# Kernel optimization log

Measured on AMD Instinct MI355X. Metric: run time of the kernel, lower is better.

The kernel has to match this reference:

```python
import jax, jax.numpy as jnp
import numpy as np
from math import pi, sqrt, factorial

NUM_SPHERICAL = 7
NUM_RADIAL = 6
CUTOFF = 5.0


def _sph_jn_np(x, n):
    # spherical Bessel j_n(x) in float64 numpy via upward recurrence
    x = np.asarray(x, dtype=np.float64)
    jm = np.sin(x) / x
    if n == 0:
        return jm
    jc = np.sin(x) / x**2 - np.cos(x) / x
    for l in range(2, n + 1):
        jm, jc = jc, (2 * l - 1) / x * jc - jm
    return jc


def _jn_zeros(n, k):
    # first k positive zeros of j_l for l = 0..n-1 (zeros of j_l interleave those of j_{l-1})
    nz = k + n
    z = np.zeros((n, nz))
    z[0] = np.arange(1, nz + 1) * np.pi
    for l in range(1, n):
        for j in range(nz - l):
            a, b = z[l - 1, j], z[l - 1, j + 1]
            fa = _sph_jn_np(a, l)
            for _ in range(100):
                m = 0.5 * (a + b)
                fm = _sph_jn_np(m, l)
                if fa * fm <= 0:
                    b = m
                else:
                    a, fa = m, fm
            z[l, j] = 0.5 * (a + b)
    return z[:, :k]


_ZEROS_NP = _jn_zeros(NUM_SPHERICAL, NUM_RADIAL)  # (n, k)
_NORM_NP = np.array([[(0.5 * _sph_jn_np(_ZEROS_NP[l, j], l + 1) ** 2) ** -0.5
                      for j in range(NUM_RADIAL)] for l in range(NUM_SPHERICAL)])
BESSEL_ZEROS = jnp.asarray(_ZEROS_NP, dtype=jnp.float32)  # z_{l,j}
BESSEL_NORM = jnp.asarray(_NORM_NP, dtype=jnp.float32)    # sqrt(2)/|j_{l+1}(z_{l,j})|


def _rbf(dist):
    # normalized spherical Bessel basis: rbf[:, l*k + j] = norm[l,j] * j_l(z_{l,j} * dist/cutoff)
    d = dist / CUTOFF
    u = d[:, None, None] * BESSEL_ZEROS[None]  # (E, n, k)
    cols = []
    for l in range(NUM_SPHERICAL):
        x = u[:, l, :]
        jm = jnp.sin(x) / x  # j_0
        if l == 0:
            jc = jm
        else:
            jc = jnp.sin(x) / (x * x) - jnp.cos(x) / x  # j_1
        for ll in range(2, l + 1):
            jm, jc = jc, (2 * ll - 1) / x * jc - jm
        cols.append(BESSEL_NORM[l] * jc)
    return jnp.concatenate(cols, axis=1)  # (E, n*k)


def _cbf(angle, phi):
    # real spherical harmonics Y_{l,m}(angle, phi), flat order m = -l..l per l
    n = NUM_SPHERICAL
    z = jnp.cos(angle)
    s = jnp.sin(angle)
    P = {(0, 0): jnp.ones_like(z)}
    for m in range(1, n):
        P[(m, m)] = (1 - 2 * m) * s * P[(m - 1, m - 1)]  # Condon-Shortley phase included
    for m in range(0, n - 1):
        P[(m + 1, m)] = (2 * m + 1) * z * P[(m, m)]
    for m in range(n):
        for l in range(m + 2, n):
            P[(l, m)] = ((2 * l - 1) * z * P[(l - 1, m)] - (l + m - 1) * P[(l - 2, m)]) / (l - m)

    def pref(l, m):
        return sqrt((2 * l + 1) * factorial(l - m) / (4.0 * pi * factorial(l + m)))

    cols = [jnp.full_like(angle, 0.5 / sqrt(pi))]  # Y_00 constant
    for l in range(1, n):
        for m in range(-l, l + 1):
            am = abs(m)
            if m < 0:
                cols.append(sqrt(2.0) * pref(l, am) * jnp.sin(am * phi) * P[(l, am)])
            elif m == 0:
                cols.append(pref(l, 0) * P[(l, 0)])
            else:
                cols.append(sqrt(2.0) * pref(l, am) * jnp.cos(am * phi) * P[(l, am)])
    return jnp.stack(cols, axis=1)  # (T, n*n)


def setup_inputs() -> dict:
    key = jax.random.key(0)
    kd, ka, kp, ki = jax.random.split(key, 4)
    E, T = 150000, 500000
    dist = jax.random.uniform(kd, (E,), minval=0.5, maxval=5.0, dtype=jnp.float32)
    angle = jax.random.uniform(ka, (T,), minval=0.0, maxval=float(np.pi), dtype=jnp.float32)
    phi = jax.random.uniform(kp, (T,), minval=-float(np.pi), maxval=float(np.pi), dtype=jnp.float32)
    idx_kj = jax.random.randint(ki, (T,), 0, E)
    return {"dist": dist, "angle": angle, "phi": phi, "idx_kj": idx_kj}


def reference(dist, angle, phi, idx_kj):
    n, k = NUM_SPHERICAL, NUM_RADIAL
    rbf = _rbf(dist)          # (E, n*k)
    cbf = _cbf(angle, phi)    # (T, n*n)
    out = (rbf[idx_kj].reshape(-1, 1, n, k) * cbf.reshape(-1, n, n, 1)).reshape(-1, n * n * k)
    return out
```

## Files before the change

kernel.cpp:

```cpp
#include <hip/hip_runtime.h>
#include <math.h>

#ifndef M_PI
#define M_PI 3.14159265358979323846
#endif

#define NS 7
#define NK 6
#define GT 64
#define BT 256
#define NC (NS*NS)
#define NR (NS*NK)
#define NF2 147

typedef float f32x2 __attribute__((ext_vector_type(2)));


__device__ double d_sph_jl(double x, int l) {
  double s = sin(x), c = cos(x);
  double j0 = s / x;
  if (l == 0) return j0;
  double j1 = s / (x * x) - c / x;
  for (int ll = 2; ll <= l; ++ll) {
    double t = (2.0 * ll - 1.0) / x * j1 - j0;
    j0 = j1; j1 = t;
  }
  return j1;
}

__global__ void setup_kernel(float* tab) {
  int id = threadIdx.x;
  if (id < NS * NK) {
    int l = id / NK, j = id % NK;
    double nu = l + 0.5;
    double mu = 4.0 * nu * nu;
    double b  = ((double)(j + 1) + 0.5 * nu - 0.25) * M_PI;
    double b8 = 8.0 * b;
    double x = b - (mu - 1.0) / b8
                 - 4.0 * (mu - 1.0) * (7.0 * mu - 31.0) / (3.0 * b8 * b8 * b8)
                 - 32.0 * (mu - 1.0) * (83.0 * mu * mu - 982.0 * mu + 3779.0) /
                   (15.0 * b8 * b8 * b8 * b8 * b8);
    for (int it = 0; it < 6; ++it) {
      double jl  = d_sph_jl(x, l);
      double jm1 = (l == 0) ? cos(x) / x : d_sph_jl(x, l - 1);
      double dj  = jm1 - (l + 1.0) / x * jl;
      x -= jl / dj;
    }
    tab[id] = (float)x;
    double jn = d_sph_jl(x, l + 1);
    tab[NS * NK + id] = (float)(sqrt(2.0) / fabs(jn));
  }
  if (id < NS * NS) {
    double v;
    if (id == 0) {
      v = 0.5 / sqrt(M_PI);
    } else {
      int l = 1;
      while ((l + 1) * (l + 1) <= id) ++l;
      int m  = id - l * l - l;
      int am = m < 0 ? -m : m;
      double fr = 1.0;
      for (int i2 = l - am + 1; i2 <= l + am; ++i2) fr *= (double)i2;
      double pref = sqrt((2.0 * l + 1.0) / (4.0 * M_PI * fr));
      v = (m != 0) ? sqrt(2.0) * pref : pref;
    }
    tab[2 * NS * NK + id] = (float)v;
  }
}

__global__ __launch_bounds__(BT, 4) void torsion_kernel(
    const float* __restrict__ dist, const float* __restrict__ angle,
    const float* __restrict__ phi, const int* __restrict__ idx_kj,
    const float* __restrict__ tab, float* __restrict__ out, int T) {
  __shared__ float s_cbf[GT][NC];
  __shared__ __align__(16) float s_rbf[GT][NR];
  __shared__ float s_d[GT];
  __shared__ float s_tab[133];
  __shared__ unsigned short s_map[NF2 + 1];

  const int tid = threadIdx.x;
  const int t0  = blockIdx.x * GT;
  const int nt  = min(GT, T - t0);

  if (tid < GT) {
    int t = t0 + tid;
    float dd = 1.0f;
    if (t < T) dd = dist[idx_kj[t]] * 0.2f;
    s_d[tid] = dd;
  }
  if (tid < 133) s_tab[tid] = tab[tid];
  if (tid < NF2) {
    int ii = tid / 21, rem2 = tid - 21 * ii, jj = rem2 / 3;
    s_map[tid] = (unsigned short)((ii * NS + jj) | (rem2 << 8));
  }
  __syncthreads();

  if (tid < GT) {
    int t = t0 + tid;
    if (t < T) {
      float a = angle[t], ph = phi[t];
      float z = cosf(a), s = sinf(a);
      float sp, cp;
      sincosf(ph, &sp, &cp);
      float cmv[NS], smv[NS];
      cmv[0] = 1.0f; smv[0] = 0.0f;
      cmv[1] = cp;   smv[1] = sp;
#pragma unroll
      for (int m = 2; m < NS; ++m) {
        cmv[m] = 2.0f * cp * cmv[m - 1] - cmv[m - 2];
        smv[m] = 2.0f * cp * smv[m - 1] - smv[m - 2];
      }
      const float* coef = s_tab + 2 * NR;
      float* crow = s_cbf[tid];
      float pmm = 1.0f;
#pragma unroll
      for (int m = 0; m < NS; ++m) {
        float pl1 = pmm, pl2 = 0.0f;
#pragma unroll
        for (int l = m; l < NS; ++l) {
          float plm;
          if (l == m)          plm = pmm;
          else if (l == m + 1) plm = (float)(2 * m + 1) * z * pmm;
          else                 plm = ((float)(2 * l - 1) * z * pl1 -
                                      (float)(l + m - 1) * pl2) *
                                     (float)(1.0 / (double)(l - m));
          int cpn = l * l + l + m;
          if (m == 0) {
            crow[cpn] = coef[cpn] * plm;
          } else {
            crow[cpn] = coef[cpn] * cmv[m] * plm;
            int cmn = l * l + l - m;
            crow[cmn] = coef[cmn] * smv[m] * plm;
          }
          pl2 = pl1; pl1 = plm;
        }
        pmm = (float)(-1 - 2 * m) * s * pmm;
      }
    }
  }

  {
    int i2 = tid;
    int t  = tid / NR;
    int cc = tid - NR * t;
    float* rlin = &s_rbf[0][0];
    while (i2 < GT * NR) {
      int l = (cc * 43) >> 8;
      float x = s_d[t] * s_tab[cc];
      float sx, cx;
      sincosf(x, &sx, &cx);
      float invx = 1.0f / x;
      float jm = sx * invx;
      float jc;
      if (l == 0) jc = jm;
      else {
        jc = (sx * invx - cx) * invx;
#pragma unroll
        for (int ll = 2; ll <= 6; ++ll) {
          if (ll <= l) {
            float tt = (float)(2 * ll - 1) * invx * jc - jm;
            jm = jc; jc = tt;
          }
        }
      }
      rlin[i2] = s_tab[NR + cc] * jc;
      i2 += BT;
      cc += 4; t += 6;
      if (cc >= NR) { cc -= NR; ++t; }
    }
  }
  __syncthreads();

  const f32x2* r2 = (const f32x2*)&s_rbf[0][0];
  f32x2* o2 = (f32x2*)out + (size_t)t0 * NF2;

  if (nt == GT) {
    int i = tid;
    int t = 0, c2 = tid;
    if (c2 >= NF2) { c2 -= NF2; t = 1; }
#pragma unroll 4
    for (int k = 0; k < 36; ++k) {
      unsigned int mp = s_map[c2];
      float cv = s_cbf[t][mp & 0xff];
      f32x2 rv = r2[t * 21 + (mp >> 8)];
      f32x2 ov = cv * rv;
      __builtin_nontemporal_store(ov, o2 + i);
      i += BT;
      c2 += 109; ++t;
      if (c2 >= NF2) { c2 -= NF2; ++t; }
    }
    if (tid < 192) {
      unsigned int mp = s_map[c2];
      float cv = s_cbf[t][mp & 0xff];
      f32x2 rv = r2[t * 21 + (mp >> 8)];
      f32x2 ov = cv * rv;
      __builtin_nontemporal_store(ov, o2 + i);
    }
  } else {
    int tot = nt * NF2;
    for (int i = tid; i < tot; i += BT) {
      int t  = i / NF2;
      int c2 = i - NF2 * t;
      unsigned int mp = s_map[c2];
      float cv = s_cbf[t][mp & 0xff];
      f32x2 rv = r2[t * 21 + (mp >> 8)];
      f32x2 ov = cv * rv;
      __builtin_nontemporal_store(ov, o2 + i);
    }
  }
}

extern "C" void kernel_launch(void* const* d_in, const int* in_sizes, int n_in,
                              void* d_out, int out_size, void* d_ws, size_t ws_size,
                              hipStream_t stream) {
  const float* dist  = (const float*)d_in[0];
  const float* angle = (const float*)d_in[1];
  const float* phi   = (const float*)d_in[2];
  const int*   idx   = (const int*)d_in[3];
  float* out = (float*)d_out;
  float* tab = (float*)d_ws;
  int T = in_sizes[1];

  hipLaunchKernelGGL(setup_kernel, dim3(1), dim3(64), 0, stream, tab);
  int nb = (T + GT - 1) / GT;
  hipLaunchKernelGGL(torsion_kernel, dim3(nb), dim3(BT), 0, stream,
                     dist, angle, phi, idx, tab, out, T);
}
```

Measured before the change: 136.5 us.

## Widen output stores to 16 bytes and split cbf/rbf work across waves

The output store loop now writes float4 (16-byte) nontemporal stores, each built from two map lookups, in place of 8-byte stores. The rbf basis computation is given to the three waves that were idle during the cbf computation, so the two phases run concurrently instead of one after the other. The angle and phi loads are hoisted ahead of the first barrier. The setup kernel reuses the j_{l-1} value for its Newton step and for the norm, runs fewer Newton iterations, and uses a second wave for the prefactors. This adds index arithmetic per store, and the reduced iteration count could affect the precision of the zeros.

```diff
diff --git a/kernel.cpp b/kernel.cpp
--- a/kernel.cpp
+++ b/kernel.cpp
@@ -14,18 +14,20 @@
 #define NF2 147
 
 typedef float f32x2 __attribute__((ext_vector_type(2)));
-
-
-__device__ double d_sph_jl(double x, int l) {
+typedef float f32x4 __attribute__((ext_vector_type(4)));
+
+
+__device__ void jl_pair(double x, int l, double& jl, double& jm1) {
   double s = sin(x), c = cos(x);
   double j0 = s / x;
-  if (l == 0) return j0;
-  double j1 = s / (x * x) - c / x;
+  double jm = c / x;
+  if (l == 0) { jl = j0; jm1 = jm; return; }
+  double j1 = (s / x - c) / x;
   for (int ll = 2; ll <= l; ++ll) {
     double t = (2.0 * ll - 1.0) / x * j1 - j0;
     j0 = j1; j1 = t;
   }
-  return j1;
+  jl = j1; jm1 = j0;
 }
 
 __global__ void setup_kernel(float* tab) {
@@ -40,31 +42,33 @@
                  - 4.0 * (mu - 1.0) * (7.0 * mu - 31.0) / (3.0 * b8 * b8 * b8)
                  - 32.0 * (mu - 1.0) * (83.0 * mu * mu - 982.0 * mu + 3779.0) /
                    (15.0 * b8 * b8 * b8 * b8 * b8);
-    for (int it = 0; it < 6; ++it) {
-      double jl  = d_sph_jl(x, l);
-      double jm1 = (l == 0) ? cos(x) / x : d_sph_jl(x, l - 1);
-      double dj  = jm1 - (l + 1.0) / x * jl;
+    double jl, jm1;
+    for (int it = 0; it < 4; ++it) {
+      jl_pair(x, l, jl, jm1);
+      double dj = jm1 - (l + 1.0) / x * jl;
       x -= jl / dj;
     }
     tab[id] = (float)x;
-    double jn = d_sph_jl(x, l + 1);
-    tab[NS * NK + id] = (float)(sqrt(2.0) / fabs(jn));
-  }
-  if (id < NS * NS) {
+    jl_pair(x, l, jl, jm1);
+    double jp1 = (2.0 * l + 1.0) / x * jl - jm1;
+    tab[NS * NK + id] = (float)(sqrt(2.0) / fabs(jp1));
+  }
+  if (id >= 64 && id < 64 + NC) {
+    int c = id - 64;
     double v;
-    if (id == 0) {
+    if (c == 0) {
       v = 0.5 / sqrt(M_PI);
     } else {
       int l = 1;
-      while ((l + 1) * (l + 1) <= id) ++l;
-      int m  = id - l * l - l;
+      while ((l + 1) * (l + 1) <= c) ++l;
+      int m  = c - l * l - l;
       int am = m < 0 ? -m : m;
       double fr = 1.0;
       for (int i2 = l - am + 1; i2 <= l + am; ++i2) fr *= (double)i2;
       double pref = sqrt((2.0 * l + 1.0) / (4.0 * M_PI * fr));
       v = (m != 0) ? sqrt(2.0) * pref : pref;
     }
-    tab[2 * NS * NK + id] = (float)v;
+    tab[2 * NS * NK + c] = (float)v;
   }
 }
 
@@ -82,10 +86,15 @@
   const int t0  = blockIdx.x * GT;
   const int nt  = min(GT, T - t0);
 
+  float a = 0.0f, ph = 0.0f;
   if (tid < GT) {
     int t = t0 + tid;
     float dd = 1.0f;
-    if (t < T) dd = dist[idx_kj[t]] * 0.2f;
+    if (t < T) {
+      dd = dist[idx_kj[t]] * 0.2f;
+      a  = angle[t];
+      ph = phi[t];
+    }
     s_d[tid] = dd;
   }
   if (tid < 133) s_tab[tid] = tab[tid];
@@ -96,9 +105,7 @@
   __syncthreads();
 
   if (tid < GT) {
-    int t = t0 + tid;
-    if (t < T) {
-      float a = angle[t], ph = phi[t];
+    if (t0 + tid < T) {
       float z = cosf(a), s = sinf(a);
       float sp, cp;
       sincosf(ph, &sp, &cp);
@@ -129,22 +136,21 @@
             crow[cpn] = coef[cpn] * plm;
           } else {
             crow[cpn] = coef[cpn] * cmv[m] * plm;
-            int cmn = l * l + l - m;
-            crow[cmn] = coef[cmn] * smv[m] * plm;
+            crow[l * l + l - m] = coef[l * l + l - m] * smv[m] * plm;
           }
           pl2 = pl1; pl1 = plm;
         }
         pmm = (float)(-1 - 2 * m) * s * pmm;
       }
     }
-  }
-
-  {
-    int i2 = tid;
-    int t  = tid / NR;
-    int cc = tid - NR * t;
+  } else {
+    int j  = tid - 64;
+    int t  = j / NR;
+    int cc = j - NR * t;
+    int i2 = j;
     float* rlin = &s_rbf[0][0];
-    while (i2 < GT * NR) {
+#pragma unroll 2
+    for (int it = 0; it < 14; ++it) {
       int l = (cc * 43) >> 8;
       float x = s_d[t] * s_tab[cc];
       float sx, cx;
@@ -164,44 +170,53 @@
         }
       }
       rlin[i2] = s_tab[NR + cc] * jc;
-      i2 += BT;
-      cc += 4; t += 6;
+      i2 += 192;
+      cc += 24; t += 4;
       if (cc >= NR) { cc -= NR; ++t; }
     }
   }
   __syncthreads();
 
   const f32x2* r2 = (const f32x2*)&s_rbf[0][0];
-  f32x2* o2 = (f32x2*)out + (size_t)t0 * NF2;
+
+  auto body = [&](int i, int p, int k, f32x4* o4) {
+    int t2 = p << 1;
+    int c2 = k << 1;
+    int toff0 = (c2 >= NF2) ? 1 : 0;
+    int cc0 = c2 - (toff0 ? NF2 : 0);
+    int ta = t2 + toff0;
+    unsigned mp0 = s_map[cc0];
+    float cv0 = s_cbf[ta][mp0 & 0xff];
+    f32x2 rv0 = r2[ta * 21 + (mp0 >> 8)];
+    int c21 = c2 + 1;
+    int toff1 = (c21 >= NF2) ? 1 : 0;
+    int cc1 = c21 - (toff1 ? NF2 : 0);
+    int tb = t2 + toff1;
+    unsigned mp1 = s_map[cc1];
+    float cv1 = s_cbf[tb][mp1 & 0xff];
+    f32x2 rv1 = r2[tb * 21 + (mp1 >> 8)];
+    f32x4 ov = {cv0 * rv0.x, cv0 * rv0.y, cv1 * rv1.x, cv1 * rv1.y};
+    __builtin_nontemporal_store(ov, o4 + i);
+  };
 
   if (nt == GT) {
-    int i = tid;
-    int t = 0, c2 = tid;
-    if (c2 >= NF2) { c2 -= NF2; t = 1; }
-#pragma unroll 4
-    for (int k = 0; k < 36; ++k) {
-      unsigned int mp = s_map[c2];
-      float cv = s_cbf[t][mp & 0xff];
-      f32x2 rv = r2[t * 21 + (mp >> 8)];
-      f32x2 ov = cv * rv;
-      __builtin_nontemporal_store(ov, o2 + i);
-      i += BT;
-      c2 += 109; ++t;
-      if (c2 >= NF2) { c2 -= NF2; ++t; }
-    }
-    if (tid < 192) {
-      unsigned int mp = s_map[c2];
-      float cv = s_cbf[t][mp & 0xff];
-      f32x2 rv = r2[t * 21 + (mp >> 8)];
-      f32x2 ov = cv * rv;
-      __builtin_nontemporal_store(ov, o2 + i);
-    }
+    f32x4* o4 = (f32x4*)out + (size_t)blockIdx.x * 4704;
+    int i = tid, p = 0, k = tid;
+    if (k >= NF2) { k -= NF2; p = 1; }
+#pragma unroll 3
+    for (int it = 0; it < 18; ++it) {
+      body(i, p, k, o4);
+      i += BT; k += 109; ++p;
+      if (k >= NF2) { k -= NF2; ++p; }
+    }
+    if (tid < 96) body(i, p, k, o4);
   } else {
+    f32x2* o2 = (f32x2*)out + (size_t)t0 * NF2;
     int tot = nt * NF2;
     for (int i = tid; i < tot; i += BT) {
       int t  = i / NF2;
       int c2 = i - NF2 * t;
-      unsigned int mp = s_map[c2];
+      unsigned mp = s_map[c2];
       float cv = s_cbf[t][mp & 0xff];
       f32x2 rv = r2[t * 21 + (mp >> 8)];
       f32x2 ov = cv * rv;
@@ -221,7 +236,7 @@
   float* tab = (float*)d_ws;
   int T = in_sizes[1];
 
-  hipLaunchKernelGGL(setup_kernel, dim3(1), dim3(64), 0, stream, tab);
+  hipLaunchKernelGGL(setup_kernel, dim3(1), dim3(128), 0, stream, tab);
   int nb = (T + GT - 1) / GT;
   hipLaunchKernelGGL(torsion_kernel, dim3(nb), dim3(BT), 0, stream,
                      dist, angle, phi, idx, tab, out, T);
```

After: 128.0 us. 1.07x faster.
